# Performance work log

Hardware: AMD Instinct MI355X
Metric: run time of the kernel (lower is better)

Reference implementation:

```python
import jax, jax.numpy as jnp
import numpy as np

B, T, E, H = 256, 200, 512, 8
NEG = -(2.0 ** 32) + 1.0  # padding value used by the TF implementation


def _pos_table(T, E):
    # sin/cos positional encoding exactly as in PositionEncoding.build
    pos = np.arange(T)[:, None].astype(np.float64)
    i = np.arange(E)[None, :]
    angle = pos / np.power(10000.0, 2.0 * (i // 2) / E)
    pe = np.where(i % 2 == 0, np.sin(angle), np.cos(angle))
    return jnp.asarray(pe, dtype=jnp.float32)


def setup_inputs() -> dict:
    key = jax.random.key(0)
    ks = jax.random.split(key, 9)
    tn = lambda k, shape, std: (jax.random.truncated_normal(k, -2.0, 2.0, shape, jnp.float32) * std)
    glorot = lambda k, shape: jax.random.uniform(k, shape, jnp.float32,
                                                 -np.sqrt(6.0 / (shape[0] + shape[1])),
                                                 np.sqrt(6.0 / (shape[0] + shape[1])))
    return {
        "queries": jax.random.normal(ks[0], (B, T, E), jnp.float32),
        "keys": jax.random.normal(ks[1], (B, T, E), jnp.float32),
        "query_len": jax.random.randint(ks[2], (B, 1), 1, T + 1),
        "key_len": jax.random.randint(ks[3], (B, 1), 1, T + 1),
        "pos_q": _pos_table(T, E),
        "pos_k": _pos_table(T, E),
        "W_Q": tn(ks[4], (E, E), 0.05),
        "W_K": tn(ks[5], (E, E), 0.05),
        "W_V": tn(ks[6], (E, E), 0.05),
        "fw1": glorot(ks[7], (E, 4 * E)),
        "fw2": glorot(ks[8], (4 * E, E)),
    }


def reference(queries, keys, query_len, key_len, pos_q, pos_k, W_Q, W_K, W_V, fw1, fw2):
    Bq, Tq, Eq = queries.shape
    Dh = Eq // H
    dt = queries.dtype
    neg = jnp.asarray(NEG, dt)

    # positional encoding: scaled table added to inputs
    scale = jnp.asarray(Eq, dt) ** 0.5
    q_in = queries + pos_q * scale          # (B,T,E)
    k_in = keys + pos_k * scale

    # sequence masks from lengths (B,1) -> (B,T)
    ar = jnp.arange(Tq)[None, :]
    q_mask = (ar < query_len).astype(dt)
    k_mask = (ar < key_len).astype(dt)

    # projections, split into heads
    Q = (q_in @ W_Q).reshape(Bq, Tq, H, Dh)
    K_ = (k_in @ W_K).reshape(Bq, Tq, H, Dh)
    V = (k_in @ W_V).reshape(Bq, Tq, H, Dh)

    # scaled dot-product attention  (B,H,Tq,Tk)
    scores = jnp.einsum('bqhd,bkhd->bhqk', Q, K_) / jnp.asarray(Dh, dt) ** 0.5
    scores = jnp.where(k_mask[:, None, None, :] > 0, scores, neg)
    # blinding: mask the diagonal (query attends to itself)
    eye = jnp.eye(Tq, dtype=bool)
    scores = jnp.where(eye[None, None], neg, scores)
    scores = scores - jnp.max(scores, axis=-1, keepdims=True)
    attn = jax.nn.softmax(scores, axis=-1)
    attn = attn * q_mask[:, None, :, None]

    out = jnp.einsum('bhqk,bkhd->bqhd', attn, V).reshape(Bq, Tq, Eq)

    # residual (use_res=True), no layer norm (use_layer_norm=False)
    out = out + q_in

    # pointwise feed-forward + residual
    ff = jax.nn.relu(out @ fw1) @ fw2
    out = out + ff

    # output_type == 'mean'
    return jnp.mean(out, axis=1, keepdims=True)  # (B,1,E)
```

## Files before the change

### kernel.cpp

```cpp
#include <hip/hip_runtime.h>

#define B_   256
#define T_   200
#define E_   512
#define H_   8
#define Dh_  64
#define F_   2048
#define M_   (B_ * T_)
#define SCALE 22.62741699796952f
#define NEGV  -4294967296.0f

typedef __attribute__((ext_vector_type(8))) short bf16x8;
typedef __attribute__((ext_vector_type(4))) float f32x4;

__device__ __forceinline__ float bf2f(unsigned short u) {
    union { unsigned u32; float f; } v; v.u32 = ((unsigned)u) << 16; return v.f;
}
__device__ __forceinline__ unsigned short f2bf(float f) {
    union { float f32; unsigned u; } v; v.f32 = f;
    unsigned r = v.u + 0x7FFFu + ((v.u >> 16) & 1u);
    return (unsigned short)(r >> 16);
}
__device__ __forceinline__ unsigned pack_hilo(float f) {
    unsigned short hi = f2bf(f);
    unsigned short lo = f2bf(f - bf2f(hi));
    return (unsigned)hi | ((unsigned)lo << 16);
}
__device__ __forceinline__ void load_lds16(const void* g, void* l) {
    __builtin_amdgcn_global_load_lds(
        (const __attribute__((address_space(1))) unsigned int*)g,
        (__attribute__((address_space(3))) unsigned int*)l, 16, 0, 0);
}

__global__ __launch_bounds__(256) void k_prep(
    float* __restrict__ q, float* __restrict__ k,
    const float* __restrict__ pos_q, const float* __restrict__ pos_k)
{
    const int z = blockIdx.y;
    float* X = z ? k : q;
    const float* Ps = z ? pos_k : pos_q;
    size_t idx = ((size_t)blockIdx.x * 256 + threadIdx.x) * 4;
    int row = (int)(idx >> 9);
    int col = (int)(idx & 511);
    int t = row % T_;
    float4 v = *(const float4*)&X[idx];
    float4 p = *(const float4*)&Ps[(size_t)t * E_ + col];
    uint4 o;
    o.x = pack_hilo(v.x + p.x * SCALE);
    o.y = pack_hilo(v.y + p.y * SCALE);
    o.z = pack_hilo(v.z + p.z * SCALE);
    o.w = pack_hilo(v.w + p.w * SCALE);
    *(uint4*)&X[idx] = o;
}

__global__ __launch_bounds__(256) void k_trw(
    const float* __restrict__ in, unsigned short* __restrict__ oh,
    unsigned short* __restrict__ ol)
{
    const int k0 = blockIdx.x * 64, n0 = blockIdx.y * 64;
    const int tid = threadIdx.x;
    __shared__ unsigned short th[64][65], tl[64][65];
#pragma unroll
    for (int i = 0; i < 16; i++) {
        int e = i * 256 + tid;
        int r = e >> 6, c = e & 63;
        float f = in[(size_t)(k0 + r) * 512 + n0 + c];
        unsigned short h = f2bf(f);
        th[r][c] = h;
        tl[r][c] = f2bf(f - bf2f(h));
    }
    __syncthreads();
#pragma unroll
    for (int i = 0; i < 16; i++) {
        int e = i * 256 + tid;
        int r = e >> 6, c = e & 63;
        oh[(size_t)(n0 + r) * 512 + k0 + c] = th[c][r];
        ol[(size_t)(n0 + r) * 512 + k0 + c] = tl[c][r];
    }
}

template<int K, int NPROD, bool SPLIT, bool FOUT>
__global__ __launch_bounds__(256) void k_projx(
    const unsigned int* __restrict__ Apk,
    const unsigned short* __restrict__ Bh,
    const unsigned short* __restrict__ Bl,
    unsigned short* __restrict__ Chi,
    unsigned short* __restrict__ Clo)
{
    const int N = 512;
    __shared__ alignas(16) unsigned int   Asp[128 * 32];
    __shared__ alignas(16) unsigned short BsH[128 * 32];
    __shared__ alignas(16) unsigned short BsL[(NPROD >= 3) ? 128 * 32 : 8];

    const int tid = threadIdx.x;
    const int w = tid >> 6, lane = tid & 63;
    const int m0 = blockIdx.x * 128, n0 = blockIdx.y * 128;
    const int mr = lane & 15, q4 = lane >> 4;

    f32x4 acc[4][4];
#pragma unroll
    for (int i = 0; i < 4; i++)
#pragma unroll
        for (int j = 0; j < 4; j++) acc[i][j] = (f32x4){0.f, 0.f, 0.f, 0.f};

    const unsigned int* gA[4];
    unsigned int* lA[4];
#pragma unroll
    for (int it = 0; it < 4; it++) {
        int c = it * 256 + tid;
        int row = c >> 3, cc = c & 7;
        gA[it] = Apk + (size_t)(m0 + row) * K + ((cc ^ (row & 7)) * 4);
        lA[it] = Asp + (size_t)(it * 256 + w * 64) * 4;
    }
    const int c0  = w * 64 + lane;
    const int c1  = 256 + c0;
    const int bm0 = c0 >> 2, bq0 = (c0 & 3) ^ ((bm0 >> 1) & 3);
    const int bm1 = c1 >> 2, bq1 = (c1 & 3) ^ ((bm1 >> 1) & 3);
    const unsigned short* gB0h = Bh + (size_t)(n0 + bm0) * K + bq0 * 8;
    const unsigned short* gB1h = Bh + (size_t)(n0 + bm1) * K + bq1 * 8;
    const unsigned short* gB0l = (NPROD >= 3) ? Bl + (size_t)(n0 + bm0) * K + bq0 * 8 : nullptr;
    const unsigned short* gB1l = (NPROD >= 3) ? Bl + (size_t)(n0 + bm1) * K + bq1 * 8 : nullptr;
    unsigned short* lB0h = BsH + (size_t)(w * 64) * 8;
    unsigned short* lB1h = BsH + (size_t)(256 + w * 64) * 8;
    unsigned short* lB0l = BsL + (size_t)(w * 64) * 8;
    unsigned short* lB1l = BsL + (size_t)(256 + w * 64) * 8;

    int cbf[4];
#pragma unroll
    for (int t4 = 0; t4 < 4; t4++) {
        int nb = (w >> 1) * 64 + t4 * 16 + mr;
        cbf[t4] = nb * 4 + (q4 ^ ((nb >> 1) & 3));
    }
    const int ra_base = (w & 1) * 64;

    for (int k0 = 0; k0 < K; k0 += 32) {
#pragma unroll
        for (int it = 0; it < 4; it++) load_lds16(gA[it] + k0, lA[it]);
        load_lds16(gB0h + k0, lB0h);
        load_lds16(gB1h + k0, lB1h);
        if (NPROD >= 3) {
            load_lds16(gB0l + k0, lB0l);
            load_lds16(gB1l + k0, lB1l);
        }
        __syncthreads();

        bf16x8 afh[4], afl[4], bgh[4], bgl[4];
#pragma unroll
        for (int t4 = 0; t4 < 4; t4++) {
            const int ra = ra_base + t4 * 16 + mr;
            const int r7 = ra & 7;
            uint4 u0 = *(const uint4*)&Asp[(size_t)(ra * 8 + ((q4 * 2) ^ r7)) * 4];
            uint4 u1 = *(const uint4*)&Asp[(size_t)(ra * 8 + ((q4 * 2 + 1) ^ r7)) * 4];
            union { unsigned u[4]; bf16x8 v; } Hh, Ll;
            Hh.u[0] = (u0.x & 0xffffu) | (u0.y << 16);
            Hh.u[1] = (u0.z & 0xffffu) | (u0.w << 16);
            Hh.u[2] = (u1.x & 0xffffu) | (u1.y << 16);
            Hh.u[3] = (u1.z & 0xffffu) | (u1.w << 16);
            afh[t4] = Hh.v;
            Ll.u[0] = (u0.x >> 16) | (u0.y & 0xffff0000u);
            Ll.u[1] = (u0.z >> 16) | (u0.w & 0xffff0000u);
            Ll.u[2] = (u1.x >> 16) | (u1.y & 0xffff0000u);
            Ll.u[3] = (u1.z >> 16) | (u1.w & 0xffff0000u);
            afl[t4] = Ll.v;
            bgh[t4] = *(const bf16x8*)&BsH[cbf[t4] * 8];
            if (NPROD >= 3) bgl[t4] = *(const bf16x8*)&BsL[cbf[t4] * 8];
        }
#pragma unroll
        for (int i = 0; i < 4; i++)
#pragma unroll
            for (int j = 0; j < 4; j++) {
                acc[i][j] = __builtin_amdgcn_mfma_f32_16x16x32_bf16(
                    afh[i], bgh[j], acc[i][j], 0, 0, 0);
                if (NPROD >= 3)
                    acc[i][j] = __builtin_amdgcn_mfma_f32_16x16x32_bf16(
                        afh[i], bgl[j], acc[i][j], 0, 0, 0);
                acc[i][j] = __builtin_amdgcn_mfma_f32_16x16x32_bf16(
                    afl[i], bgh[j], acc[i][j], 0, 0, 0);
            }
        __syncthreads();
    }

#pragma unroll
    for (int i = 0; i < 4; i++) {
        int row = m0 + (w & 1) * 64 + i * 16 + (lane >> 4) * 4;
#pragma unroll
        for (int j = 0; j < 4; j++) {
            int col = n0 + (w >> 1) * 64 + j * 16 + mr;
#pragma unroll
            for (int r = 0; r < 4; r++) {
                float v = acc[i][j][r];
                if (FOUT) {
                    ((float*)Chi)[(size_t)(row + r) * N + col] = v;
                } else {
                    unsigned short hi = f2bf(v);
                    Chi[(size_t)(row + r) * N + col] = hi;
                    if (SPLIT)
                        Clo[(size_t)(row + r) * N + col] = f2bf(v - bf2f(hi));
                }
            }
        }
    }
}

__global__ __launch_bounds__(512, 4) void k_attn_flash(
    const unsigned short* __restrict__ Qhi, const unsigned short* __restrict__ Qlo,
    const unsigned short* __restrict__ Khi, const unsigned short* __restrict__ Klo,
    const int* __restrict__ qlen, const int* __restrict__ klen,
    const unsigned int* __restrict__ Apk,
    unsigned short* VX)
{
    const int bh = blockIdx.x;
    const int b = bh >> 3, h = bh & 7;
    const int tid = threadIdx.x;
    const int w = tid >> 6, l = tid & 63;
    const int mr = l & 15, q4 = l >> 4;

    __shared__ alignas(16) unsigned short Kh_s[2][64 * 72];
    __shared__ alignas(16) unsigned short Kl_s[2][64 * 72];
    __shared__ alignas(16) unsigned short Vt_s[2][64 * 72];
    __shared__ alignas(16) unsigned short P_s[8][16 * 72];

    const int kl = klen[b], ql = qlen[b];
    const int cmax = (kl > 1) ? ((kl + 63) >> 6) : 4;

    auto stage = [&](int cs, int sb) {
#pragma unroll
        for (int ii = 0; ii < 2; ii++) {
            const int idx = ii * 512 + tid;
            const int jn = idx >> 4, dq = idx & 15;
            const int n = cs * 64 + jn;
            if (n < T_) {
                const size_t g = (size_t)(b * T_ + n) * E_ + h * 64 + dq * 4;
                *(uint2*)&Kh_s[sb][jn * 72 + dq * 4] = *(const uint2*)&Khi[g];
                *(uint2*)&Kl_s[sb][jn * 72 + dq * 4] = *(const uint2*)&Klo[g];
                ushort4 v = *(const ushort4*)&VX[g];
                Vt_s[sb][(dq * 4 + 0) * 72 + jn] = v.x;
                Vt_s[sb][(dq * 4 + 1) * 72 + jn] = v.y;
                Vt_s[sb][(dq * 4 + 2) * 72 + jn] = v.z;
                Vt_s[sb][(dq * 4 + 3) * 72 + jn] = v.w;
            } else {
                Vt_s[sb][(dq * 4 + 0) * 72 + jn] = 0;
                Vt_s[sb][(dq * 4 + 1) * 72 + jn] = 0;
                Vt_s[sb][(dq * 4 + 2) * 72 + jn] = 0;
                Vt_s[sb][(dq * 4 + 3) * 72 + jn] = 0;
            }
        }
    };

    bf16x8 qh0[2], qh1[2];
#pragma unroll
    for (int j = 0; j < 2; j++) {
        const int qt = w + 8 * j;
        if (qt < 13 && qt * 16 < ql) {
            const size_t qoff = (size_t)(b * T_ + qt * 16 + mr) * E_ + h * 64 + q4 * 8;
            qh0[j] = *(const bf16x8*)&Qhi[qoff];
            qh1[j] = *(const bf16x8*)&Qhi[qoff + 32];
        }
    }

    f32x4 O[2][4];
    float m_r[2][4], l_r[2][4];
#pragma unroll
    for (int j = 0; j < 2; j++) {
#pragma unroll
        for (int nt = 0; nt < 4; nt++) O[j][nt] = (f32x4){0.f, 0.f, 0.f, 0.f};
#pragma unroll
        for (int r = 0; r < 4; r++) { m_r[j][r] = -INFINITY; l_r[j][r] = 0.f; }
    }

    stage(0, 0);
    __syncthreads();

    for (int c = 0; c < cmax; c++) {
        const int pb = c & 1;
        if (c + 1 < cmax) stage(c + 1, pb ^ 1);

#pragma unroll
        for (int j = 0; j < 2; j++) {
            const int qt = w + 8 * j;
            if (qt < 13 && qt * 16 < ql) {
                const int q0 = qt * 16;
                const size_t qoff = (size_t)(b * T_ + q0 + mr) * E_ + h * 64 + q4 * 8;
                bf16x8 qe0 = *(const bf16x8*)&Qlo[qoff];
                bf16x8 qe1 = *(const bf16x8*)&Qlo[qoff + 32];

                f32x4 a[4];
#pragma unroll
                for (int kt = 0; kt < 4; kt++) a[kt] = (f32x4){0.f, 0.f, 0.f, 0.f};
                __builtin_amdgcn_s_setprio(1);
#pragma unroll
                for (int kt = 0; kt < 4; kt++) {
                    if (c * 64 + kt * 16 < 208) {
                        const int rbase = (kt * 16 + mr) * 72 + q4 * 8;
                        bf16x8 kh0 = *(const bf16x8*)&Kh_s[pb][rbase];
                        bf16x8 kh1 = *(const bf16x8*)&Kh_s[pb][rbase + 32];
                        bf16x8 ke0 = *(const bf16x8*)&Kl_s[pb][rbase];
                        bf16x8 ke1 = *(const bf16x8*)&Kl_s[pb][rbase + 32];
                        a[kt] = __builtin_amdgcn_mfma_f32_16x16x32_bf16(qh0[j], kh0, a[kt], 0, 0, 0);
                        a[kt] = __builtin_amdgcn_mfma_f32_16x16x32_bf16(qh1[j], kh1, a[kt], 0, 0, 0);
                        a[kt] = __builtin_amdgcn_mfma_f32_16x16x32_bf16(qh0[j], ke0, a[kt], 0, 0, 0);
                        a[kt] = __builtin_amdgcn_mfma_f32_16x16x32_bf16(qh1[j], ke1, a[kt], 0, 0, 0);
                        a[kt] = __builtin_amdgcn_mfma_f32_16x16x32_bf16(qe0, kh0, a[kt], 0, 0, 0);
                        a[kt] = __builtin_amdgcn_mfma_f32_16x16x32_bf16(qe1, kh1, a[kt], 0, 0, 0);
                    }
                }
                __builtin_amdgcn_s_setprio(0);

                float mc[4] = {-INFINITY, -INFINITY, -INFINITY, -INFINITY};
#pragma unroll
                for (int kt = 0; kt < 4; kt++) {
                    int col = c * 64 + kt * 16 + mr;
#pragma unroll
                    for (int r = 0; r < 4; r++) {
                        int row = q0 + q4 * 4 + r;
                        float v = a[kt][r] * 0.125f;
                        if (col >= kl)  v = NEGV;
                        if (col == row) v = NEGV;
                        if (col >= T_)  v = -INFINITY;
                        a[kt][r] = v;
                        mc[r] = fmaxf(mc[r], v);
                    }
                }
#pragma unroll
                for (int r = 0; r < 4; r++)
#pragma unroll
                    for (int off = 1; off < 16; off <<= 1)
                        mc[r] = fmaxf(mc[r], __shfl_xor(mc[r], off));
                float mn[4], alpha[4], ps[4];
#pragma unroll
                for (int r = 0; r < 4; r++) {
                    mn[r] = fmaxf(m_r[j][r], mc[r]);
                    alpha[r] = __expf(m_r[j][r] - mn[r]);
                    ps[r] = 0.f;
                }
#pragma unroll
                for (int kt = 0; kt < 4; kt++)
#pragma unroll
                    for (int r = 0; r < 4; r++) {
                        float p = __expf(a[kt][r] - mn[r]);
                        a[kt][r] = p;
                        ps[r] += p;
                    }
#pragma unroll
                for (int r = 0; r < 4; r++)
#pragma unroll
                    for (int off = 1; off < 16; off <<= 1)
                        ps[r] += __shfl_xor(ps[r], off);
#pragma unroll
                for (int r = 0; r < 4; r++) {
                    l_r[j][r] = l_r[j][r] * alpha[r] + ps[r];
                    m_r[j][r] = mn[r];
                }
#pragma unroll
                for (int nt = 0; nt < 4; nt++)
#pragma unroll
                    for (int r = 0; r < 4; r++) O[j][nt][r] *= alpha[r];
#pragma unroll
                for (int kt = 0; kt < 4; kt++)
#pragma unroll
                    for (int r = 0; r < 4; r++)
                        P_s[w][(q4 * 4 + r) * 72 + kt * 16 + mr] = f2bf(a[kt][r]);
                __builtin_amdgcn_s_setprio(1);
#pragma unroll
                for (int k2 = 0; k2 < 2; k2++) {
                    bf16x8 pf = *(const bf16x8*)&P_s[w][mr * 72 + k2 * 32 + q4 * 8];
#pragma unroll
                    for (int nt = 0; nt < 4; nt++) {
                        bf16x8 vf = *(const bf16x8*)&Vt_s[pb][(nt * 16 + mr) * 72 + k2 * 32 + q4 * 8];
                        O[j][nt] = __builtin_amdgcn_mfma_f32_16x16x32_bf16(pf, vf, O[j][nt], 0, 0, 0);
                    }
                }
                __builtin_amdgcn_s_setprio(0);
            }
        }
        __syncthreads();
    }

#pragma unroll
    for (int j = 0; j < 2; j++) {
        const int qt = w + 8 * j;
        if (qt < 13) {
#pragma unroll
            for (int r = 0; r < 4; r++) {
                int row = qt * 16 + q4 * 4 + r;
                if (row < T_) {
                    float inv = (row < ql) ? (1.f / l_r[j][r]) : 0.f;
#pragma unroll
                    for (int nt = 0; nt < 4; nt++) {
                        int d = nt * 16 + mr;
                        size_t gi = (size_t)(b * T_ + row) * E_ + h * 64 + d;
                        unsigned u = Apk[gi];
                        float res = bf2f((unsigned short)(u & 0xffff)) +
                                    bf2f((unsigned short)(u >> 16));
                        VX[gi] = f2bf(O[j][nt][r] * inv + res);
                    }
                }
            }
        }
    }
}

__global__ __launch_bounds__(256) void k_tr(
    const float* __restrict__ in, unsigned short* __restrict__ out, int K, int N)
{
    const int k0 = blockIdx.x * 64, n0 = blockIdx.y * 64;
    const int tid = threadIdx.x;
    __shared__ unsigned short t[64][65];
#pragma unroll
    for (int i = 0; i < 16; i++) {
        int e = i * 256 + tid;
        int r = e >> 6, c = e & 63;
        t[r][c] = f2bf(in[(size_t)(k0 + r) * N + n0 + c]);
    }
    __syncthreads();
#pragma unroll
    for (int i = 0; i < 16; i++) {
        int e = i * 256 + tid;
        int r = e >> 6, c = e & 63;
        out[(size_t)(n0 + r) * K + k0 + c] = t[c][r];
    }
}

__global__ __launch_bounds__(256) void k_gemm_relusum(
    const unsigned short* __restrict__ A,
    const unsigned short* __restrict__ Bt,
    float* __restrict__ Hsum)
{
    const int K = E_, N = F_;
    __shared__ alignas(16) unsigned short As[128 * 32];
    __shared__ alignas(16) unsigned short Bs[128 * 32];
    __shared__ float colsum[2][128];

    const int tid  = threadIdx.x;
    const int w    = tid >> 6, lane = tid & 63;
    const int m0   = blockIdx.x * 128, n0 = blockIdx.y * 128;
    const int mr   = lane & 15, q = lane >> 4;

    f32x4 acc[4][4];
#pragma unroll
    for (int i = 0; i < 4; i++)
#pragma unroll
        for (int j = 0; j < 4; j++) acc[i][j] = (f32x4){0.f, 0.f, 0.f, 0.f};

    const int c0  = w * 64 + lane;
    const int c1  = 256 + w * 64 + lane;
    const int am0 = c0 >> 2, aq0 = (c0 & 3) ^ ((am0 >> 1) & 3);
    const int am1 = c1 >> 2, aq1 = (c1 & 3) ^ ((am1 >> 1) & 3);
    const unsigned short* gA0 = A  + (size_t)(m0 + am0) * K + aq0 * 8;
    const unsigned short* gA1 = A  + (size_t)(m0 + am1) * K + aq1 * 8;
    const unsigned short* gB0 = Bt + (size_t)(n0 + am0) * K + aq0 * 8;
    const unsigned short* gB1 = Bt + (size_t)(n0 + am1) * K + aq1 * 8;
    unsigned short* lA0 = As + (size_t)(w * 64) * 8;
    unsigned short* lA1 = As + (size_t)(256 + w * 64) * 8;
    unsigned short* lB0 = Bs + (size_t)(w * 64) * 8;
    unsigned short* lB1 = Bs + (size_t)(256 + w * 64) * 8;

    int caf[4], cbf[4];
#pragma unroll
    for (int t4 = 0; t4 < 4; t4++) {
        int ma = (w & 1) * 64 + t4 * 16 + mr;
        caf[t4] = ma * 4 + (q ^ ((ma >> 1) & 3));
        int nb = (w >> 1) * 64 + t4 * 16 + mr;
        cbf[t4] = nb * 4 + (q ^ ((nb >> 1) & 3));
    }

    for (int k0 = 0; k0 < K; k0 += 32) {
        load_lds16(gA0 + k0, lA0);
        load_lds16(gA1 + k0, lA1);
        load_lds16(gB0 + k0, lB0);
        load_lds16(gB1 + k0, lB1);
        __syncthreads();

        bf16x8 af[4], bg[4];
#pragma unroll
        for (int t4 = 0; t4 < 4; t4++) {
            af[t4] = *(const bf16x8*)&As[caf[t4] * 8];
            bg[t4] = *(const bf16x8*)&Bs[cbf[t4] * 8];
        }
#pragma unroll
        for (int i = 0; i < 4; i++)
#pragma unroll
            for (int j = 0; j < 4; j++)
                acc[i][j] = __builtin_amdgcn_mfma_f32_16x16x32_bf16(
                    af[i], bg[j], acc[i][j], 0, 0, 0);
        __syncthreads();
    }

    ((float*)colsum)[tid] = 0.f;
    __syncthreads();
    const int b0 = m0 / 200;
    const int bsplit = (b0 + 1) * 200;
#pragma unroll
    for (int j = 0; j < 4; j++) {
        const int colr = (w >> 1) * 64 + j * 16 + mr;
        float s0 = 0.f, s1 = 0.f;
#pragma unroll
        for (int i = 0; i < 4; i++) {
            const int rowb = m0 + (w & 1) * 64 + i * 16 + q * 4;
#pragma unroll
            for (int r = 0; r < 4; r++) {
                float v = fmaxf(acc[i][j][r], 0.f);
                if (rowb + r >= bsplit) s1 += v; else s0 += v;
            }
        }
        atomicAdd(&colsum[0][colr], s0);
        atomicAdd(&colsum[1][colr], s1);
    }
    __syncthreads();
    if (tid < 128) {
        atomicAdd(&Hsum[(size_t)b0 * N + n0 + tid], colsum[0][tid]);
        if (bsplit < m0 + 128)
            atomicAdd(&Hsum[(size_t)(b0 + 1) * N + n0 + tid], colsum[1][tid]);
    }
}

__global__ __launch_bounds__(256) void k_zero(float* __restrict__ p)
{
    ((float4*)p)[(size_t)blockIdx.x * 256 + threadIdx.x] = (float4){0.f, 0.f, 0.f, 0.f};
}

__global__ __launch_bounds__(256) void k_hm(
    const float* __restrict__ Hsum, unsigned int* __restrict__ Hmpk)
{
    size_t idx = ((size_t)blockIdx.x * 256 + threadIdx.x) * 4;
    float4 v = *(const float4*)&Hsum[idx];
    uint4 o;
    o.x = pack_hilo(v.x * (1.0f / 200.0f));
    o.y = pack_hilo(v.y * (1.0f / 200.0f));
    o.z = pack_hilo(v.z * (1.0f / 200.0f));
    o.w = pack_hilo(v.w * (1.0f / 200.0f));
    *(uint4*)&Hmpk[idx] = o;
}

__global__ __launch_bounds__(256) void k_final(
    const unsigned short* __restrict__ X, const float* __restrict__ ffm,
    float* __restrict__ out)
{
    const int b = blockIdx.x;
    const int w = threadIdx.x >> 6, lane = threadIdx.x & 63;
    float s[8] = {0.f, 0.f, 0.f, 0.f, 0.f, 0.f, 0.f, 0.f};
    for (int t = w; t < T_; t += 4) {
        bf16x8 v = *(const bf16x8*)&X[(size_t)(b * T_ + t) * E_ + lane * 8];
#pragma unroll
        for (int j = 0; j < 8; j++) s[j] += bf2f((unsigned short)v[j]);
    }
    __shared__ float red[4][512];
#pragma unroll
    for (int j = 0; j < 8; j++) red[w][lane * 8 + j] = s[j];
    __syncthreads();
    for (int e = threadIdx.x; e < 512; e += 256)
        out[(size_t)b * E_ + e] =
            (red[0][e] + red[1][e] + red[2][e] + red[3][e]) * (1.0f / 200.0f) +
            ffm[(size_t)b * E_ + e];
}

extern "C" void kernel_launch(void* const* d_in, const int* in_sizes, int n_in,
                              void* d_out, int out_size, void* d_ws, size_t ws_size,
                              hipStream_t stream)
{
    float* qmut = (float*)d_in[0];
    float* kmut = (float*)d_in[1];
    const int*   qlen  = (const int*)d_in[2];
    const int*   klen  = (const int*)d_in[3];
    const float* pos_q = (const float*)d_in[4];
    const float* pos_k = (const float*)d_in[5];
    const float* W_Q   = (const float*)d_in[6];
    const float* W_K   = (const float*)d_in[7];
    const float* W_V   = (const float*)d_in[8];
    const float* fw1   = (const float*)d_in[9];
    const float* fw2   = (const float*)d_in[10];
    float* out = (float*)d_out;

    char* base = (char*)d_ws;
    unsigned short* Qhi = (unsigned short*)base;
    unsigned short* Qlo = (unsigned short*)(base +  52428800);
    unsigned short* Khi = (unsigned short*)(base + 104857600);
    unsigned short* Klo = (unsigned short*)(base + 157286400);
    unsigned short* VX  = (unsigned short*)(base + 209715200);

    unsigned short* wQh = VX;
    unsigned short* wQl = VX + 262144;
    unsigned short* wKh = VX + 524288;
    unsigned short* wKl = VX + 786432;
    unsigned short* wVh = (unsigned short*)W_Q;
    unsigned short* wVl = (unsigned short*)W_Q + 262144;

    unsigned short* fw1t = (unsigned short*)(base + 157286400);
    unsigned short* fw2t = (unsigned short*)(base + 159383552);
    float*        Hsum = (float*)(base + 161480704);
    unsigned int* Hmpk = (unsigned int*)(base + 163577856);
    float*        ffm  = (float*)(base + 165675008);

    const unsigned int* Aq = (const unsigned int*)qmut;
    const unsigned int* Ak = (const unsigned int*)kmut;

    k_prep<<<dim3(M_ * E_ / 1024, 2), 256, 0, stream>>>(qmut, kmut, pos_q, pos_k);
    k_trw<<<dim3(8, 8), 256, 0, stream>>>(W_Q, wQh, wQl);
    k_trw<<<dim3(8, 8), 256, 0, stream>>>(W_K, wKh, wKl);
    k_projx<512, 3, true, false><<<dim3(M_ / 128, 4), 256, 0, stream>>>(
        Aq, wQh, wQl, Qhi, Qlo);
    k_projx<512, 3, true, false><<<dim3(M_ / 128, 4), 256, 0, stream>>>(
        Ak, wKh, wKl, Khi, Klo);
    k_trw<<<dim3(8, 8), 256, 0, stream>>>(W_V, wVh, wVl);
    k_projx<512, 2, false, false><<<dim3(M_ / 128, 4), 256, 0, stream>>>(
        Ak, wVh, nullptr, VX, nullptr);

    k_attn_flash<<<B_ * H_, 512, 0, stream>>>(
        Qhi, Qlo, Khi, Klo, qlen, klen, Aq, VX);

    k_tr<<<dim3(E_ / 64, F_ / 64), 256, 0, stream>>>(fw1, fw1t, E_, F_);
    k_tr<<<dim3(F_ / 64, E_ / 64), 256, 0, stream>>>(fw2, fw2t, F_, E_);
    k_zero<<<512, 256, 0, stream>>>(Hsum);

    k_gemm_relusum<<<dim3(M_ / 128, F_ / 128), 256, 0, stream>>>(VX, fw1t, Hsum);
    k_hm<<<512, 256, 0, stream>>>(Hsum, Hmpk);
    k_projx<2048, 2, false, true><<<dim3(2, 4), 256, 0, stream>>>(
        Hmpk, fw2t, nullptr, (unsigned short*)ffm, nullptr);
    k_final<<<B_, 256, 0, stream>>>(VX, ffm, out);
}
```

Baseline: 923.6 us.

## Skip padded-row projection tiles, swap grid order, double K-step in FFN GEMM

Projection GEMM tiles whose 128 rows all fall beyond the sequence length of a single batch are now zero-filled and exit early instead of computing. For V the skip applies only when the key length is greater than 1. The grid axes of the projection and FFN GEMMs are swapped so neighbouring blocks share the same A rows, which should improve L2 reuse. The FFN GEMM also loads 64 K-elements per barrier pair using two LDS buffers, halving the number of synchronisations. The risk is correctness: zeroed Q/K/V rows must match what the attention kernel assumes about masked positions, and the V rows feed the residual path.

```diff
diff --git a/kernel.cpp b/kernel.cpp
--- a/kernel.cpp
+++ b/kernel.cpp
@@ -79,13 +79,14 @@
     }
 }
 
-template<int K, int NPROD, bool SPLIT, bool FOUT>
+template<int K, int NPROD, bool SPLIT, bool FOUT, int SKIPM>
 __global__ __launch_bounds__(256) void k_projx(
     const unsigned int* __restrict__ Apk,
     const unsigned short* __restrict__ Bh,
     const unsigned short* __restrict__ Bl,
     unsigned short* __restrict__ Chi,
-    unsigned short* __restrict__ Clo)
+    unsigned short* __restrict__ Clo,
+    const int* __restrict__ slen)
 {
     const int N = 512;
     __shared__ alignas(16) unsigned int   Asp[128 * 32];
@@ -94,8 +95,30 @@
 
     const int tid = threadIdx.x;
     const int w = tid >> 6, lane = tid & 63;
-    const int m0 = blockIdx.x * 128, n0 = blockIdx.y * 128;
+    const int m0 = blockIdx.y * 128, n0 = blockIdx.x * 128;
     const int mr = lane & 15, q4 = lane >> 4;
+
+    if (SKIPM) {
+        const int bA = m0 / 200;
+        const int bB = (m0 + 127) / 200;
+        if (bA == bB) {
+            const int len = slen[bA];
+            const int t0 = m0 - bA * 200;
+            if (t0 >= len && (SKIPM == 1 || len > 1)) {
+#pragma unroll
+                for (int i = 0; i < 8; i++) {
+                    int e = i * 256 + tid;
+                    int r = e >> 4, cc = e & 15;
+                    *(uint4*)&Chi[(size_t)(m0 + r) * N + n0 + cc * 8] =
+                        (uint4){0u, 0u, 0u, 0u};
+                    if (SPLIT)
+                        *(uint4*)&Clo[(size_t)(m0 + r) * N + n0 + cc * 8] =
+                            (uint4){0u, 0u, 0u, 0u};
+                }
+                return;
+            }
+        }
+    }
 
     f32x4 acc[4][4];
 #pragma unroll
@@ -427,13 +450,13 @@
     float* __restrict__ Hsum)
 {
     const int K = E_, N = F_;
-    __shared__ alignas(16) unsigned short As[128 * 32];
-    __shared__ alignas(16) unsigned short Bs[128 * 32];
+    __shared__ alignas(16) unsigned short As[2][128 * 32];
+    __shared__ alignas(16) unsigned short Bs[2][128 * 32];
     __shared__ float colsum[2][128];
 
     const int tid  = threadIdx.x;
     const int w    = tid >> 6, lane = tid & 63;
-    const int m0   = blockIdx.x * 128, n0 = blockIdx.y * 128;
+    const int m0   = blockIdx.y * 128, n0 = blockIdx.x * 128;
     const int mr   = lane & 15, q = lane >> 4;
 
     f32x4 acc[4][4];
@@ -450,10 +473,10 @@
     const unsigned short* gA1 = A  + (size_t)(m0 + am1) * K + aq1 * 8;
     const unsigned short* gB0 = Bt + (size_t)(n0 + am0) * K + aq0 * 8;
     const unsigned short* gB1 = Bt + (size_t)(n0 + am1) * K + aq1 * 8;
-    unsigned short* lA0 = As + (size_t)(w * 64) * 8;
-    unsigned short* lA1 = As + (size_t)(256 + w * 64) * 8;
-    unsigned short* lB0 = Bs + (size_t)(w * 64) * 8;
-    unsigned short* lB1 = Bs + (size_t)(256 + w * 64) * 8;
+    unsigned short* lA0[2] = { As[0] + (size_t)(w * 64) * 8, As[1] + (size_t)(w * 64) * 8 };
+    unsigned short* lA1[2] = { As[0] + (size_t)(256 + w * 64) * 8, As[1] + (size_t)(256 + w * 64) * 8 };
+    unsigned short* lB0[2] = { Bs[0] + (size_t)(w * 64) * 8, Bs[1] + (size_t)(w * 64) * 8 };
+    unsigned short* lB1[2] = { Bs[0] + (size_t)(256 + w * 64) * 8, Bs[1] + (size_t)(256 + w * 64) * 8 };
 
     int caf[4], cbf[4];
 #pragma unroll
@@ -464,25 +487,31 @@
         cbf[t4] = nb * 4 + (q ^ ((nb >> 1) & 3));
     }
 
-    for (int k0 = 0; k0 < K; k0 += 32) {
-        load_lds16(gA0 + k0, lA0);
-        load_lds16(gA1 + k0, lA1);
-        load_lds16(gB0 + k0, lB0);
-        load_lds16(gB1 + k0, lB1);
+    for (int k0 = 0; k0 < K; k0 += 64) {
+#pragma unroll
+        for (int hh = 0; hh < 2; hh++) {
+            load_lds16(gA0 + k0 + hh * 32, lA0[hh]);
+            load_lds16(gA1 + k0 + hh * 32, lA1[hh]);
+            load_lds16(gB0 + k0 + hh * 32, lB0[hh]);
+            load_lds16(gB1 + k0 + hh * 32, lB1[hh]);
+        }
         __syncthreads();
 
-        bf16x8 af[4], bg[4];
-#pragma unroll
-        for (int t4 = 0; t4 < 4; t4++) {
-            af[t4] = *(const bf16x8*)&As[caf[t4] * 8];
-            bg[t4] = *(const bf16x8*)&Bs[cbf[t4] * 8];
-        }
-#pragma unroll
-        for (int i = 0; i < 4; i++)
-#pragma unroll
-            for (int j = 0; j < 4; j++)
-                acc[i][j] = __builtin_amdgcn_mfma_f32_16x16x32_bf16(
-                    af[i], bg[j], acc[i][j], 0, 0, 0);
+#pragma unroll
+        for (int hh = 0; hh < 2; hh++) {
+            bf16x8 af[4], bg[4];
+#pragma unroll
+            for (int t4 = 0; t4 < 4; t4++) {
+                af[t4] = *(const bf16x8*)&As[hh][caf[t4] * 8];
+                bg[t4] = *(const bf16x8*)&Bs[hh][cbf[t4] * 8];
+            }
+#pragma unroll
+            for (int i = 0; i < 4; i++)
+#pragma unroll
+                for (int j = 0; j < 4; j++)
+                    acc[i][j] = __builtin_amdgcn_mfma_f32_16x16x32_bf16(
+                        af[i], bg[j], acc[i][j], 0, 0, 0);
+        }
         __syncthreads();
     }
 
@@ -597,13 +626,13 @@
     k_prep<<<dim3(M_ * E_ / 1024, 2), 256, 0, stream>>>(qmut, kmut, pos_q, pos_k);
     k_trw<<<dim3(8, 8), 256, 0, stream>>>(W_Q, wQh, wQl);
     k_trw<<<dim3(8, 8), 256, 0, stream>>>(W_K, wKh, wKl);
-    k_projx<512, 3, true, false><<<dim3(M_ / 128, 4), 256, 0, stream>>>(
-        Aq, wQh, wQl, Qhi, Qlo);
-    k_projx<512, 3, true, false><<<dim3(M_ / 128, 4), 256, 0, stream>>>(
-        Ak, wKh, wKl, Khi, Klo);
+    k_projx<512, 3, true, false, 1><<<dim3(4, M_ / 128), 256, 0, stream>>>(
+        Aq, wQh, wQl, Qhi, Qlo, qlen);
+    k_projx<512, 3, true, false, 1><<<dim3(4, M_ / 128), 256, 0, stream>>>(
+        Ak, wKh, wKl, Khi, Klo, klen);
     k_trw<<<dim3(8, 8), 256, 0, stream>>>(W_V, wVh, wVl);
-    k_projx<512, 2, false, false><<<dim3(M_ / 128, 4), 256, 0, stream>>>(
-        Ak, wVh, nullptr, VX, nullptr);
+    k_projx<512, 2, false, false, 2><<<dim3(4, M_ / 128), 256, 0, stream>>>(
+        Ak, wVh, nullptr, VX, nullptr, klen);
 
     k_attn_flash<<<B_ * H_, 512, 0, stream>>>(
         Qhi, Qlo, Khi, Klo, qlen, klen, Aq, VX);
@@ -612,9 +641,9 @@
     k_tr<<<dim3(F_ / 64, E_ / 64), 256, 0, stream>>>(fw2, fw2t, F_, E_);
     k_zero<<<512, 256, 0, stream>>>(Hsum);
 
-    k_gemm_relusum<<<dim3(M_ / 128, F_ / 128), 256, 0, stream>>>(VX, fw1t, Hsum);
+    k_gemm_relusum<<<dim3(F_ / 128, M_ / 128), 256, 0, stream>>>(VX, fw1t, Hsum);
     k_hm<<<512, 256, 0, stream>>>(Hsum, Hmpk);
-    k_projx<2048, 2, false, true><<<dim3(2, 4), 256, 0, stream>>>(
-        Hmpk, fw2t, nullptr, (unsigned short*)ffm, nullptr);
+    k_projx<2048, 2, false, true, 0><<<dim3(4, 2), 256, 0, stream>>>(
+        Hmpk, fw2t, nullptr, (unsigned short*)ffm, nullptr, nullptr);
     k_final<<<B_, 256, 0, stream>>>(VX, ffm, out);
 }
```

Result: slower. 954.9 us (+3.4%).
